# Kernel tuning notes

Measured on AMD Instinct MI355X. Metric: run time of the kernel, lower is better.

Reference implementation:

```python
import jax, jax.numpy as jnp
import numpy as np

RADIUS = 0.1
MAX_EDGES = 4_194_304  # cap on total neighbor pairs (expected ~1.1M)

def _cdist(a, b):
    # pairwise Euclidean distances: [M,3] x [N,3] -> [M,N]
    a2 = jnp.sum(a * a, axis=-1, keepdims=True)          # [M,1]
    b2 = jnp.sum(b * b, axis=-1, keepdims=True).T        # [1,N]
    d2 = a2 + b2 - 2.0 * (a @ b.T)
    return jnp.sqrt(jnp.maximum(d2, 0.0))


def setup_inputs() -> dict:
    key = jax.random.key(0)
    k1, k2 = jax.random.split(key)
    inp_positions = jax.random.uniform(k1, (16384, 3), dtype=jnp.float32)
    out_positions = jax.random.uniform(k2, (16384, 3), dtype=jnp.float32)
    return {"inp_positions": inp_positions, "out_positions": out_positions}


def reference(inp_positions, out_positions):
    M = out_positions.shape[0]
    N = inp_positions.shape[0]
    distances = _cdist(out_positions, inp_positions)      # [M,N]
    mask = distances <= RADIUS                            # [M,N] bool
    # jit-compatible nonzero: flatten, fixed-size output, sentinel fill M*N
    flat_idx = jnp.nonzero(mask.ravel(), size=MAX_EDGES, fill_value=M * N)[0]
    query_index = flat_idx // N                           # padded slots -> M (out of range sentinel)
    neighbors_index = jnp.where(flat_idx < M * N, flat_idx % N, -1)
    # bincount(query_index, minlength=M) == row-wise sum of mask
    counts = jnp.sum(mask, axis=1)                        # [M] int32
    row_splits = jnp.pad(jnp.cumsum(counts), (1, 0))      # [M+1]
    return neighbors_index, row_splits
```

## Files before the change

kernel.cpp:

```cpp
#include <hip/hip_runtime.h>
#include <math.h>

constexpr int M_ROWS    = 16384;
constexpr int N_PTS     = 16384;
constexpr int MAX_EDGES = 4194304;

constexpr int GD     = 10;
constexpr int NCELLS = GD * GD * GD;
constexpr int NBLK   = N_PTS / 256;
constexpr int NK     = 27;
constexpr int NTH    = NK * M_ROWS;
constexpr int KGRID  = NTH / 256;
constexpr int NSCANB = M_ROWS / 256;

static __device__ __forceinline__ int cell_coord(float v) {
    int c = (int)(v * 10.0f);
    return c < 0 ? 0 : (c > GD - 1 ? GD - 1 : c);
}

__global__ void __launch_bounds__(256)
bin_hist_kernel(const float* __restrict__ inp, const float* __restrict__ outp,
                float4* __restrict__ aq, int* __restrict__ H,
                int* __restrict__ counter, float T) {
    int b = blockIdx.x, t = threadIdx.x;
    if (b == 0 && t == 0) *counter = 0;
    __shared__ int h[NCELLS];
    for (int i = t; i < NCELLS; i += 256) h[i] = 0;
    __syncthreads();
    int j = b * 256 + t;
    float x = inp[j * 3 + 0], y = inp[j * 3 + 1], z = inp[j * 3 + 2];
    int cid = (cell_coord(x) * GD + cell_coord(y)) * GD + cell_coord(z);
    atomicAdd(&h[cid], 1);
    float qx = outp[j * 3 + 0], qy = outp[j * 3 + 1], qz = outp[j * 3 + 2];
    float w = __fadd_rn(__fadd_rn(__fmul_rn(qx, qx), __fmul_rn(qy, qy)), __fmul_rn(qz, qz));
    aq[j] = make_float4(qx, qy, qz, __fsub_rn(T, w));
    __syncthreads();
    for (int i = t; i < NCELLS; i += 256) H[b * NCELLS + i] = h[i];
}

__global__ void __launch_bounds__(1024)
scan_cells_kernel(int* __restrict__ H, int* __restrict__ cellStart) {
    __shared__ int sc[1024];
    int c = threadIdx.x;
    int tot = 0;
    if (c < NCELLS) {
        for (int b = 0; b < NBLK; ++b) {
            int v = H[b * NCELLS + c];
            H[b * NCELLS + c] = tot;
            tot += v;
        }
    }
    sc[c] = tot;
    __syncthreads();
    for (int off = 1; off < 1024; off <<= 1) {
        int v = (c >= off) ? sc[c - off] : 0;
        __syncthreads();
        sc[c] += v;
        __syncthreads();
    }
    if (c <= NCELLS) cellStart[c] = (c == 0) ? 0 : sc[c - 1];
}

__global__ void __launch_bounds__(256)
scatter_kernel(const float* __restrict__ inp, const int* __restrict__ H,
               const int* __restrict__ cellStart, float4* __restrict__ sortedB,
               int* __restrict__ sortedJ) {
    int b = blockIdx.x, t = threadIdx.x;
    int j = b * 256 + t;
    float x = inp[j * 3 + 0], y = inp[j * 3 + 1], z = inp[j * 3 + 2];
    int cid = (cell_coord(x) * GD + cell_coord(y)) * GD + cell_coord(z);
    __shared__ int scid[256];
    scid[t] = cid;
    __syncthreads();
    int rank = 0;
    for (int i = 0; i < 255; ++i)
        if (i < t) rank += (scid[i] == cid);
    int pos = cellStart[cid] + H[b * NCELLS + cid] + rank;
    float s = __fadd_rn(__fadd_rn(__fmul_rn(x, x), __fmul_rn(y, y)), __fmul_rn(z, z));
    sortedB[pos] = make_float4(-2.0f * x, -2.0f * y, -2.0f * z, s);
    sortedJ[pos] = j;
}

__global__ void __launch_bounds__(256)
count_kernel(const float4* __restrict__ aq, const float4* __restrict__ sortedB,
             const int* __restrict__ cellStart, unsigned char* __restrict__ cnt27) {
    int t = blockIdx.x * 256 + threadIdx.x;
    int k = t >> 14, row = t & (M_ROWS - 1);
    float4 a = aq[row];
    int cx = cell_coord(a.x) + (k / 9) - 1;
    int cy = cell_coord(a.y) + ((k / 3) % 3) - 1;
    int cz = cell_coord(a.z) + (k % 3) - 1;
    int cnt = 0;
    if (((unsigned)cx < GD) & ((unsigned)cy < GD) & ((unsigned)cz < GD)) {
        int cid = (cx * GD + cy) * GD + cz;
        int s = cellStart[cid], e = cellStart[cid + 1];
        for (int p = s; p < e; ++p) {
            float4 q = sortedB[p];
            float v = __fmaf_rn(a.x, q.x, __fmaf_rn(a.y, q.y, __fmaf_rn(a.z, q.z, q.w)));
            cnt += (v <= a.w);
        }
    }
    cnt27[t] = (unsigned char)cnt;
}

__global__ void __launch_bounds__(256)
scan_rows_kernel(const unsigned char* __restrict__ cnt27, unsigned short* __restrict__ cpfx27,
                 int* __restrict__ totals, int* __restrict__ row_splits,
                 int* __restrict__ counter) {
    __shared__ int sp[256];
    __shared__ int lastflag;
    int t = threadIdx.x;
    int row = blockIdx.x * 256 + t;
    int sum = 0;
#pragma unroll
    for (int k = 0; k < NK; ++k) {
        cpfx27[k * M_ROWS + row] = (unsigned short)sum;
        sum += cnt27[k * M_ROWS + row];
    }
    totals[row] = sum;
    __threadfence();
    if (t == 0) lastflag = (atomicAdd(counter, 1) == NSCANB - 1);
    __syncthreads();
    if (!lastflag) return;
    __threadfence();

    const int4* t4 = (const int4*)totals;
    int s = 0;
#pragma unroll
    for (int i = 0; i < 16; ++i) {
        int4 v = t4[t * 16 + i];
        s += v.x + v.y + v.z + v.w;
    }
    sp[t] = s;
    __syncthreads();
    for (int off = 1; off < 256; off <<= 1) {
        int v = (t >= off) ? sp[t - off] : 0;
        __syncthreads();
        sp[t] += v;
        __syncthreads();
    }
    int cur = (t == 0) ? 0 : sp[t - 1];
#pragma unroll
    for (int i = 0; i < 16; ++i) {
        int4 v = t4[t * 16 + i];
        row_splits[t * 64 + i * 4 + 0] = cur; cur += v.x;
        row_splits[t * 64 + i * 4 + 1] = cur; cur += v.y;
        row_splits[t * 64 + i * 4 + 2] = cur; cur += v.z;
        row_splits[t * 64 + i * 4 + 3] = cur; cur += v.w;
    }
    if (t == 255) row_splits[M_ROWS] = sp[255];
}

__global__ void __launch_bounds__(256)
emit_fill_kernel(const float4* __restrict__ aq, const float4* __restrict__ sortedB,
                 const int* __restrict__ sortedJ, const int* __restrict__ cellStart,
                 const unsigned short* __restrict__ cpfx27, const int* __restrict__ rs,
                 int* __restrict__ out_idx) {
    int t = blockIdx.x * 256 + threadIdx.x;
    int k = t >> 14, row = t & (M_ROWS - 1);
    float4 a = aq[row];
    int cx = cell_coord(a.x) + (k / 9) - 1;
    int cy = cell_coord(a.y) + ((k / 3) % 3) - 1;
    int cz = cell_coord(a.z) + (k % 3) - 1;
    if (((unsigned)cx < GD) & ((unsigned)cy < GD) & ((unsigned)cz < GD)) {
        int cid = (cx * GD + cy) * GD + cz;
        int s = cellStart[cid], e = cellStart[cid + 1];
        int cur = rs[row] + (int)cpfx27[k * M_ROWS + row];
        for (int p = s; p < e; ++p) {
            float4 q = sortedB[p];
            float v = __fmaf_rn(a.x, q.x, __fmaf_rn(a.y, q.y, __fmaf_rn(a.z, q.z, q.w)));
            if (v <= a.w) out_idx[cur++] = sortedJ[p];
        }
    }
    int E = rs[M_ROWS];
    int total = MAX_EDGES - E;
    if (total > 0) {
        int per = (total + KGRID - 1) / KGRID;
        int s0  = E + blockIdx.x * per;
        int e0  = s0 + per; if (e0 > MAX_EDGES) e0 = MAX_EDGES;
        for (int i = s0 + threadIdx.x; i < e0; i += 256) out_idx[i] = -1;
    }
}

extern "C" void kernel_launch(void* const* d_in, const int* in_sizes, int n_in,
                              void* d_out, int out_size, void* d_ws, size_t ws_size,
                              hipStream_t stream) {
    const float* inp  = (const float*)d_in[0];
    const float* outp = (const float*)d_in[1];
    int* out_idx    = (int*)d_out;
    int* row_splits = out_idx + MAX_EDGES;

    char* ws = (char*)d_ws;
    size_t off = 0;
    float4* aq      = (float4*)(ws + off); off += (size_t)M_ROWS * 16;
    float4* sortedB = (float4*)(ws + off); off += (size_t)N_PTS * 16;
    int*    sortedJ = (int*)(ws + off);    off += (size_t)N_PTS * 4;
    int*    H       = (int*)(ws + off);    off += (size_t)NBLK * NCELLS * 4;
    int*    cellStart = (int*)(ws + off);  off += 1024 * 4;
    unsigned char*  cnt27  = (unsigned char*)(ws + off);  off += (size_t)NTH;
    unsigned short* cpfx27 = (unsigned short*)(ws + off); off += (size_t)NTH * 2;
    int* totals  = (int*)(ws + off); off += (size_t)M_ROWS * 4;
    int* counter = (int*)(ws + off); off += 256;
    if (off > ws_size) return;

    double md = (double)0.1f + ldexp(1.0, -28);
    double m2 = md * md;
    float  T  = (float)m2;
    if ((double)T >= m2) T = nextafterf(T, 0.0f);

    bin_hist_kernel <<<dim3(NBLK),  dim3(256),  0, stream>>>(inp, outp, aq, H, counter, T);
    scan_cells_kernel<<<dim3(1),    dim3(1024), 0, stream>>>(H, cellStart);
    scatter_kernel  <<<dim3(NBLK),  dim3(256),  0, stream>>>(inp, H, cellStart, sortedB, sortedJ);
    count_kernel    <<<dim3(KGRID), dim3(256),  0, stream>>>(aq, sortedB, cellStart, cnt27);
    scan_rows_kernel<<<dim3(NSCANB),dim3(256),  0, stream>>>(cnt27, cpfx27, totals, row_splits, counter);
    emit_fill_kernel<<<dim3(KGRID), dim3(256),  0, stream>>>(aq, sortedB, sortedJ, cellStart, cpfx27, row_splits, out_idx);
}
```

Measured before the change: 90.86 us.

## Sort query points by cell and fuse cell scan into histogram kernel

Query points are now binned and sorted by grid cell just like the input points, so threads in a wavefront scan the same neighbor cells. This reduces divergence and improves cache reuse in the count and emit kernels. The separate single-block cell scan kernel is folded into the histogram kernel through a last-block-done counter, and the counters are reset with a memset. The costs are an extra scatter of the queries, an indirection through sortedRow when writing totals and reading row offsets, and a serial last-block scan over both histograms.

```diff
diff --git a/kernel.cpp b/kernel.cpp
--- a/kernel.cpp
+++ b/kernel.cpp
@@ -17,83 +17,115 @@
     int c = (int)(v * 10.0f);
     return c < 0 ? 0 : (c > GD - 1 ? GD - 1 : c);
 }
-
-__global__ void __launch_bounds__(256)
-bin_hist_kernel(const float* __restrict__ inp, const float* __restrict__ outp,
-                float4* __restrict__ aq, int* __restrict__ H,
-                int* __restrict__ counter, float T) {
+static __device__ __forceinline__ int cell_id(float x, float y, float z) {
+    return (cell_coord(x) * GD + cell_coord(y)) * GD + cell_coord(z);
+}
+
+__global__ void __launch_bounds__(256)
+hist_kernel(const float* __restrict__ inp, const float* __restrict__ outp,
+            int* __restrict__ HB, int* __restrict__ HA,
+            int* __restrict__ cellStartB, int* __restrict__ cellStartA,
+            int* __restrict__ counter) {
+    __shared__ int hb[NCELLS], ha[NCELLS];
+    __shared__ int sB[256], sA[256];
+    __shared__ int lastflag;
     int b = blockIdx.x, t = threadIdx.x;
-    if (b == 0 && t == 0) *counter = 0;
-    __shared__ int h[NCELLS];
-    for (int i = t; i < NCELLS; i += 256) h[i] = 0;
+    for (int i = t; i < NCELLS; i += 256) { hb[i] = 0; ha[i] = 0; }
     __syncthreads();
     int j = b * 256 + t;
-    float x = inp[j * 3 + 0], y = inp[j * 3 + 1], z = inp[j * 3 + 2];
-    int cid = (cell_coord(x) * GD + cell_coord(y)) * GD + cell_coord(z);
-    atomicAdd(&h[cid], 1);
-    float qx = outp[j * 3 + 0], qy = outp[j * 3 + 1], qz = outp[j * 3 + 2];
-    float w = __fadd_rn(__fadd_rn(__fmul_rn(qx, qx), __fmul_rn(qy, qy)), __fmul_rn(qz, qz));
-    aq[j] = make_float4(qx, qy, qz, __fsub_rn(T, w));
-    __syncthreads();
-    for (int i = t; i < NCELLS; i += 256) H[b * NCELLS + i] = h[i];
-}
-
-__global__ void __launch_bounds__(1024)
-scan_cells_kernel(int* __restrict__ H, int* __restrict__ cellStart) {
-    __shared__ int sc[1024];
-    int c = threadIdx.x;
-    int tot = 0;
-    if (c < NCELLS) {
-        for (int b = 0; b < NBLK; ++b) {
-            int v = H[b * NCELLS + c];
-            H[b * NCELLS + c] = tot;
-            tot += v;
-        }
-    }
-    sc[c] = tot;
-    __syncthreads();
-    for (int off = 1; off < 1024; off <<= 1) {
-        int v = (c >= off) ? sc[c - off] : 0;
-        __syncthreads();
-        sc[c] += v;
-        __syncthreads();
-    }
-    if (c <= NCELLS) cellStart[c] = (c == 0) ? 0 : sc[c - 1];
-}
-
-__global__ void __launch_bounds__(256)
-scatter_kernel(const float* __restrict__ inp, const int* __restrict__ H,
-               const int* __restrict__ cellStart, float4* __restrict__ sortedB,
-               int* __restrict__ sortedJ) {
+    atomicAdd(&hb[cell_id(inp[j * 3 + 0], inp[j * 3 + 1], inp[j * 3 + 2])], 1);
+    atomicAdd(&ha[cell_id(outp[j * 3 + 0], outp[j * 3 + 1], outp[j * 3 + 2])], 1);
+    __syncthreads();
+    for (int i = t; i < NCELLS; i += 256) {
+        HB[i * NBLK + b] = hb[i];
+        HA[i * NBLK + b] = ha[i];
+    }
+    __threadfence();
+    if (t == 0) lastflag = (atomicAdd(counter, 1) == NBLK - 1);
+    __syncthreads();
+    if (!lastflag) return;
+    __threadfence();
+    int tb[4], ta[4];
+#pragma unroll
+    for (int q = 0; q < 4; ++q) {
+        int c = t * 4 + q, rb = 0, ra = 0;
+        if (c < NCELLS) {
+            for (int k = 0; k < NBLK; ++k) {
+                int v = HB[c * NBLK + k]; HB[c * NBLK + k] = rb; rb += v;
+            }
+            for (int k = 0; k < NBLK; ++k) {
+                int v = HA[c * NBLK + k]; HA[c * NBLK + k] = ra; ra += v;
+            }
+        }
+        tb[q] = rb; ta[q] = ra;
+    }
+    int pb[4], pa[4], rb = 0, ra = 0;
+#pragma unroll
+    for (int q = 0; q < 4; ++q) { pb[q] = rb; rb += tb[q]; pa[q] = ra; ra += ta[q]; }
+    sB[t] = rb; sA[t] = ra;
+    __syncthreads();
+    for (int off = 1; off < 256; off <<= 1) {
+        int vb = (t >= off) ? sB[t - off] : 0;
+        int va = (t >= off) ? sA[t - off] : 0;
+        __syncthreads();
+        sB[t] += vb; sA[t] += va;
+        __syncthreads();
+    }
+    int eb = (t == 0) ? 0 : sB[t - 1];
+    int ea = (t == 0) ? 0 : sA[t - 1];
+#pragma unroll
+    for (int q = 0; q < 4; ++q) {
+        int c = t * 4 + q;
+        if (c < NCELLS) { cellStartB[c] = eb + pb[q]; cellStartA[c] = ea + pa[q]; }
+    }
+    if (t == 255) { cellStartB[NCELLS] = sB[255]; cellStartA[NCELLS] = sA[255]; }
+}
+
+__global__ void __launch_bounds__(256)
+scatter_kernel(const float* __restrict__ inp, const float* __restrict__ outp,
+               const int* __restrict__ HB, const int* __restrict__ HA,
+               const int* __restrict__ cellStartB, const int* __restrict__ cellStartA,
+               float4* __restrict__ sortedB, int* __restrict__ sortedJ,
+               float4* __restrict__ sortedA, int* __restrict__ sortedRow, float T) {
+    __shared__ int scB[256], scA[256];
     int b = blockIdx.x, t = threadIdx.x;
     int j = b * 256 + t;
-    float x = inp[j * 3 + 0], y = inp[j * 3 + 1], z = inp[j * 3 + 2];
-    int cid = (cell_coord(x) * GD + cell_coord(y)) * GD + cell_coord(z);
-    __shared__ int scid[256];
-    scid[t] = cid;
-    __syncthreads();
-    int rank = 0;
-    for (int i = 0; i < 255; ++i)
-        if (i < t) rank += (scid[i] == cid);
-    int pos = cellStart[cid] + H[b * NCELLS + cid] + rank;
-    float s = __fadd_rn(__fadd_rn(__fmul_rn(x, x), __fmul_rn(y, y)), __fmul_rn(z, z));
-    sortedB[pos] = make_float4(-2.0f * x, -2.0f * y, -2.0f * z, s);
-    sortedJ[pos] = j;
-}
-
-__global__ void __launch_bounds__(256)
-count_kernel(const float4* __restrict__ aq, const float4* __restrict__ sortedB,
-             const int* __restrict__ cellStart, unsigned char* __restrict__ cnt27) {
+    float bx = inp[j * 3 + 0], by = inp[j * 3 + 1], bz = inp[j * 3 + 2];
+    float qx = outp[j * 3 + 0], qy = outp[j * 3 + 1], qz = outp[j * 3 + 2];
+    int cidB = cell_id(bx, by, bz);
+    int cidA = cell_id(qx, qy, qz);
+    scB[t] = cidB; scA[t] = cidA;
+    __syncthreads();
+    int rkB = 0, rkA = 0;
+    for (int i = 0; i < 255; ++i) {
+        if (i < t) {
+            rkB += (scB[i] == cidB);
+            rkA += (scA[i] == cidA);
+        }
+    }
+    float sb2 = __fadd_rn(__fadd_rn(__fmul_rn(bx, bx), __fmul_rn(by, by)), __fmul_rn(bz, bz));
+    int posB = cellStartB[cidB] + HB[cidB * NBLK + b] + rkB;
+    sortedB[posB] = make_float4(-2.0f * bx, -2.0f * by, -2.0f * bz, sb2);
+    sortedJ[posB] = j;
+    float sa2 = __fadd_rn(__fadd_rn(__fmul_rn(qx, qx), __fmul_rn(qy, qy)), __fmul_rn(qz, qz));
+    int posA = cellStartA[cidA] + HA[cidA * NBLK + b] + rkA;
+    sortedA[posA] = make_float4(qx, qy, qz, __fsub_rn(T, sa2));
+    sortedRow[posA] = j;
+}
+
+__global__ void __launch_bounds__(256)
+count_kernel(const float4* __restrict__ sortedA, const float4* __restrict__ sortedB,
+             const int* __restrict__ cellStartB, unsigned char* __restrict__ cnt27) {
     int t = blockIdx.x * 256 + threadIdx.x;
-    int k = t >> 14, row = t & (M_ROWS - 1);
-    float4 a = aq[row];
+    int k = t >> 14, qi = t & (M_ROWS - 1);
+    float4 a = sortedA[qi];
     int cx = cell_coord(a.x) + (k / 9) - 1;
     int cy = cell_coord(a.y) + ((k / 3) % 3) - 1;
     int cz = cell_coord(a.z) + (k % 3) - 1;
     int cnt = 0;
     if (((unsigned)cx < GD) & ((unsigned)cy < GD) & ((unsigned)cz < GD)) {
         int cid = (cx * GD + cy) * GD + cz;
-        int s = cellStart[cid], e = cellStart[cid + 1];
+        int s = cellStartB[cid], e = cellStartB[cid + 1];
         for (int p = s; p < e; ++p) {
             float4 q = sortedB[p];
             float v = __fmaf_rn(a.x, q.x, __fmaf_rn(a.y, q.y, __fmaf_rn(a.z, q.z, q.w)));
@@ -104,20 +136,20 @@
 }
 
 __global__ void __launch_bounds__(256)
-scan_rows_kernel(const unsigned char* __restrict__ cnt27, unsigned short* __restrict__ cpfx27,
-                 int* __restrict__ totals, int* __restrict__ row_splits,
-                 int* __restrict__ counter) {
+qscan_kernel(const unsigned char* __restrict__ cnt27, unsigned short* __restrict__ cpfx27,
+             const int* __restrict__ sortedRow, int* __restrict__ totals,
+             int* __restrict__ row_splits, int* __restrict__ counter) {
     __shared__ int sp[256];
     __shared__ int lastflag;
     int t = threadIdx.x;
-    int row = blockIdx.x * 256 + t;
+    int qi = blockIdx.x * 256 + t;
     int sum = 0;
 #pragma unroll
     for (int k = 0; k < NK; ++k) {
-        cpfx27[k * M_ROWS + row] = (unsigned short)sum;
-        sum += cnt27[k * M_ROWS + row];
-    }
-    totals[row] = sum;
+        cpfx27[k * M_ROWS + qi] = (unsigned short)sum;
+        sum += cnt27[k * M_ROWS + qi];
+    }
+    totals[sortedRow[qi]] = sum;
     __threadfence();
     if (t == 0) lastflag = (atomicAdd(counter, 1) == NSCANB - 1);
     __syncthreads();
@@ -152,20 +184,20 @@
 }
 
 __global__ void __launch_bounds__(256)
-emit_fill_kernel(const float4* __restrict__ aq, const float4* __restrict__ sortedB,
-                 const int* __restrict__ sortedJ, const int* __restrict__ cellStart,
-                 const unsigned short* __restrict__ cpfx27, const int* __restrict__ rs,
-                 int* __restrict__ out_idx) {
+emit_fill_kernel(const float4* __restrict__ sortedA, const float4* __restrict__ sortedB,
+                 const int* __restrict__ sortedJ, const int* __restrict__ sortedRow,
+                 const int* __restrict__ cellStartB, const unsigned short* __restrict__ cpfx27,
+                 const int* __restrict__ rs, int* __restrict__ out_idx) {
     int t = blockIdx.x * 256 + threadIdx.x;
-    int k = t >> 14, row = t & (M_ROWS - 1);
-    float4 a = aq[row];
+    int k = t >> 14, qi = t & (M_ROWS - 1);
+    float4 a = sortedA[qi];
     int cx = cell_coord(a.x) + (k / 9) - 1;
     int cy = cell_coord(a.y) + ((k / 3) % 3) - 1;
     int cz = cell_coord(a.z) + (k % 3) - 1;
     if (((unsigned)cx < GD) & ((unsigned)cy < GD) & ((unsigned)cz < GD)) {
         int cid = (cx * GD + cy) * GD + cz;
-        int s = cellStart[cid], e = cellStart[cid + 1];
-        int cur = rs[row] + (int)cpfx27[k * M_ROWS + row];
+        int s = cellStartB[cid], e = cellStartB[cid + 1];
+        int cur = rs[sortedRow[qi]] + (int)cpfx27[k * M_ROWS + qi];
         for (int p = s; p < e; ++p) {
             float4 q = sortedB[p];
             float v = __fmaf_rn(a.x, q.x, __fmaf_rn(a.y, q.y, __fmaf_rn(a.z, q.z, q.w)));
@@ -192,11 +224,14 @@
 
     char* ws = (char*)d_ws;
     size_t off = 0;
-    float4* aq      = (float4*)(ws + off); off += (size_t)M_ROWS * 16;
     float4* sortedB = (float4*)(ws + off); off += (size_t)N_PTS * 16;
-    int*    sortedJ = (int*)(ws + off);    off += (size_t)N_PTS * 4;
-    int*    H       = (int*)(ws + off);    off += (size_t)NBLK * NCELLS * 4;
-    int*    cellStart = (int*)(ws + off);  off += 1024 * 4;
+    float4* sortedA = (float4*)(ws + off); off += (size_t)M_ROWS * 16;
+    int* sortedJ    = (int*)(ws + off);    off += (size_t)N_PTS * 4;
+    int* sortedRow  = (int*)(ws + off);    off += (size_t)M_ROWS * 4;
+    int* HB         = (int*)(ws + off);    off += (size_t)NCELLS * NBLK * 4;
+    int* HA         = (int*)(ws + off);    off += (size_t)NCELLS * NBLK * 4;
+    int* cellStartB = (int*)(ws + off);    off += 1024 * 4;
+    int* cellStartA = (int*)(ws + off);    off += 1024 * 4;
     unsigned char*  cnt27  = (unsigned char*)(ws + off);  off += (size_t)NTH;
     unsigned short* cpfx27 = (unsigned short*)(ws + off); off += (size_t)NTH * 2;
     int* totals  = (int*)(ws + off); off += (size_t)M_ROWS * 4;
@@ -208,10 +243,12 @@
     float  T  = (float)m2;
     if ((double)T >= m2) T = nextafterf(T, 0.0f);
 
-    bin_hist_kernel <<<dim3(NBLK),  dim3(256),  0, stream>>>(inp, outp, aq, H, counter, T);
-    scan_cells_kernel<<<dim3(1),    dim3(1024), 0, stream>>>(H, cellStart);
-    scatter_kernel  <<<dim3(NBLK),  dim3(256),  0, stream>>>(inp, H, cellStart, sortedB, sortedJ);
-    count_kernel    <<<dim3(KGRID), dim3(256),  0, stream>>>(aq, sortedB, cellStart, cnt27);
-    scan_rows_kernel<<<dim3(NSCANB),dim3(256),  0, stream>>>(cnt27, cpfx27, totals, row_splits, counter);
-    emit_fill_kernel<<<dim3(KGRID), dim3(256),  0, stream>>>(aq, sortedB, sortedJ, cellStart, cpfx27, row_splits, out_idx);
-}
+    hipMemsetAsync(counter, 0, 8, stream);
+    hist_kernel    <<<dim3(NBLK),  dim3(256), 0, stream>>>(inp, outp, HB, HA, cellStartB, cellStartA, counter);
+    scatter_kernel <<<dim3(NBLK),  dim3(256), 0, stream>>>(inp, outp, HB, HA, cellStartB, cellStartA,
+                                                           sortedB, sortedJ, sortedA, sortedRow, T);
+    count_kernel   <<<dim3(KGRID), dim3(256), 0, stream>>>(sortedA, sortedB, cellStartB, cnt27);
+    qscan_kernel   <<<dim3(NSCANB),dim3(256), 0, stream>>>(cnt27, cpfx27, sortedRow, totals, row_splits, counter + 1);
+    emit_fill_kernel<<<dim3(KGRID),dim3(256), 0, stream>>>(sortedA, sortedB, sortedJ, sortedRow,
+                                                           cellStartB, cpfx27, row_splits, out_idx);
+}
```

After: 115.9 us. +27.5%, slower.
